# Optimization experiments

Hardware: AMD Instinct MI355X
Metric: run time of the kernel (lower is better)

Reference implementation:

```python
import jax, jax.numpy as jnp
import numpy as np

HIDDEN = 4096
N_HEADS = 16
HEAD_DIM = HIDDEN // N_HEADS  # 256
ROTARY_DIM = 64
ROPE_THETA = 10000.0


def _rope_cos_sin(positions):
    # positions: [S] int -> cos/sin: [S, ROTARY_DIM//2]
    inv_freq = 1.0 / (ROPE_THETA ** (jnp.arange(0, ROTARY_DIM, 2, dtype=jnp.float32) / ROTARY_DIM))
    angles = positions.astype(jnp.float32)[:, None] * inv_freq[None, :]
    return jnp.cos(angles), jnp.sin(angles)


def _apply_rope_interleaved(x, cos, sin):
    # x: [B, S, H, D]; rotate first ROTARY_DIM dims, GPT-J (non-neox) interleaved pairs
    xr = x[..., :ROTARY_DIM]
    x1 = xr[..., 0::2]
    x2 = xr[..., 1::2]
    c = cos[None, :, None, :]
    s = sin[None, :, None, :]
    o1 = x1 * c - x2 * s
    o2 = x1 * s + x2 * c
    rot = jnp.stack([o1, o2], axis=-1).reshape(xr.shape)
    return jnp.concatenate([rot, x[..., ROTARY_DIM:]], axis=-1)


def setup_inputs() -> dict:
    key = jax.random.key(0)
    k1, k2, k3 = jax.random.split(key, 3)
    B, S = 2, 2048
    hidden_states = jax.random.normal(k1, (B, S, HIDDEN), dtype=jnp.float32)
    positions = jnp.arange(S, dtype=jnp.int32)
    w_qkv = jax.random.normal(k2, (3 * HIDDEN, HIDDEN), dtype=jnp.float32) * 0.02
    w_out = jax.random.normal(k3, (HIDDEN, HIDDEN), dtype=jnp.float32) * 0.02
    return {"hidden_states": hidden_states, "positions": positions, "w_qkv": w_qkv, "w_out": w_out}


def reference(hidden_states, positions, w_qkv, w_out):
    B, S, H = hidden_states.shape
    qkv = jnp.einsum("bsh,oh->bso", hidden_states, w_qkv)  # [B,S,3H]
    q, k, v = jnp.split(qkv, 3, axis=-1)
    q = q.reshape(B, S, N_HEADS, HEAD_DIM)
    k = k.reshape(B, S, N_HEADS, HEAD_DIM)
    v = v.reshape(B, S, N_HEADS, HEAD_DIM)
    cos, sin = _rope_cos_sin(positions)
    q = _apply_rope_interleaved(q, cos, sin)
    k = _apply_rope_interleaved(k, cos, sin)
    scale = HEAD_DIM ** -0.5
    scores = jnp.einsum("bqhd,bkhd->bhqk", q, k) * scale  # [B,nh,S,S]
    causal = jnp.tril(jnp.ones((S, S), dtype=bool))
    scores = jnp.where(causal[None, None], scores, jnp.finfo(scores.dtype).min)
    probs = jax.nn.softmax(scores, axis=-1)
    attn = jnp.einsum("bhqk,bkhd->bqhd", probs, v).reshape(B, S, H)
    return jnp.einsum("bsh,oh->bso", attn, w_out)
```

## Files before the change

### kernel.cpp

```cpp
#include <hip/hip_runtime.h>

typedef __attribute__((ext_vector_type(8))) short short8;
typedef __attribute__((ext_vector_type(4))) float f32x4;

__device__ __forceinline__ unsigned short f2bf(float f) {
    union { float f; unsigned int u; } v; v.f = f;
    unsigned int u = v.u;
    unsigned int r = (u + 0x7FFFu + ((u >> 16) & 1u)) >> 16;
    return (unsigned short)r;
}
__device__ __forceinline__ float bf2f(unsigned short u) {
    union { unsigned int u; float f; } v; v.u = ((unsigned int)u) << 16;
    return v.f;
}
__device__ __forceinline__ void load_lds16(const void* g, void* l) {
    __builtin_amdgcn_global_load_lds(
        (const __attribute__((address_space(1))) void*)g,
        (__attribute__((address_space(3))) void*)l, 16, 0, 0);
}
#define BAR() asm volatile("s_barrier" ::: "memory")
#define WAITV(n) asm volatile("s_waitcnt vmcnt(" #n ")" ::: "memory")

__device__ __forceinline__ int swz(int o) { return o ^ ((o >> 3) & 0x70); }

__global__ __launch_bounds__(256) void conv_bf16(const float* __restrict__ in,
                                                 unsigned short* __restrict__ out, int n4) {
    int i = blockIdx.x * 256 + threadIdx.x;
    if (i >= n4) return;
    float4 v = ((const float4*)in)[i];
    ushort4 o;
    o.x = f2bf(v.x); o.y = f2bf(v.y); o.z = f2bf(v.z); o.w = f2bf(v.w);
    ((ushort4*)out)[i] = o;
}

template <bool OUT_BF16>
__global__ __launch_bounds__(512, 2) void gemm256(const unsigned short* __restrict__ A,
                                                  const unsigned short* __restrict__ B,
                                                  void* __restrict__ Cv,
                                                  int M, int N, int K, int NBN) {
    __shared__ __align__(16) char smem[131072];
    const int tid = threadIdx.x;
    const int lane = tid & 63, wv = tid >> 6;
    const int wm = wv >> 2, wn = wv & 3;
    const int fr = lane & 15, fo = (lane >> 4) * 8;

    const int nwg = gridDim.x, bid = blockIdx.x;
    const int q = nwg >> 3, r = nwg & 7, xcd = bid & 7, lid = bid >> 3;
    const int wg = (xcd < r ? xcd * (q + 1) : r * (q + 1) + (xcd - r) * q) + lid;
    const int bm = wg / NBN, bn = wg % NBN;

    const unsigned short* gA = A + (size_t)bm * 256 * K;
    const unsigned short* gB = B + (size_t)bn * 256 * K;

    int srow[2][2], scol[2][2];
#pragma unroll
    for (int h = 0; h < 2; ++h)
#pragma unroll
        for (int rr = 0; rr < 2; ++rr) {
            int o = h * 16384 + rr * 8192 + tid * 16;
            int osw = swz(o);
            srow[h][rr] = osw >> 7;
            scol[h][rr] = (osw & 127) >> 1;
        }

    f32x4 acc[8][4] = {};
    short8 a[4][2], b[4][2];

    auto STAGE = [&](const unsigned short* g, int regionBase, int h, int t) {
#pragma unroll
        for (int rr = 0; rr < 2; ++rr)
            load_lds16(g + (size_t)srow[h][rr] * K + t * 64 + scol[h][rr],
                       smem + regionBase + h * 16384 + rr * 8192 + tid * 16);
    };
    auto RDA = [&](int bufBase, int mh) {
#pragma unroll
        for (int mf = 0; mf < 4; ++mf)
#pragma unroll
            for (int ks = 0; ks < 2; ++ks) {
                int o = swz((wm * 128 + mh * 64 + mf * 16 + fr) * 128 + (ks * 32 + fo) * 2);
                a[mf][ks] = *(const short8*)(smem + bufBase + o);
            }
    };
    auto RDB = [&](int bufBase, int nh) {
#pragma unroll
        for (int jj = 0; jj < 2; ++jj)
#pragma unroll
            for (int ks = 0; ks < 2; ++ks) {
                int o = swz((wn * 64 + (nh * 2 + jj) * 16 + fr) * 128 + (ks * 32 + fo) * 2);
                b[nh * 2 + jj][ks] = *(const short8*)(smem + bufBase + 32768 + o);
            }
    };
    auto MM = [&](int mh, int nh) {
        __builtin_amdgcn_s_setprio(1);
#pragma unroll
        for (int mf = 0; mf < 4; ++mf)
#pragma unroll
            for (int jj = 0; jj < 2; ++jj)
#pragma unroll
                for (int ks = 0; ks < 2; ++ks)
                    acc[mh * 4 + mf][nh * 2 + jj] = __builtin_amdgcn_mfma_f32_16x16x32_bf16(
                        a[mf][ks], b[nh * 2 + jj][ks], acc[mh * 4 + mf][nh * 2 + jj], 0, 0, 0);
        __builtin_amdgcn_s_setprio(0);
    };

    const int A0 = 0, B0 = 32768, A1 = 65536, B1 = 98304;

    STAGE(gA, A0, 0, 0); STAGE(gA, A0, 1, 0);
    STAGE(gB, B0, 0, 0); STAGE(gB, B0, 1, 0);
    STAGE(gB, B1, 0, 1); STAGE(gB, B1, 1, 1);
    STAGE(gA, A1, 0, 1); STAGE(gA, A1, 1, 1);
    WAITV(8);
    BAR();
    RDA(A0, 0);
    RDB(A0, 0);

    const int NIT = K >> 7;
    for (int i = 0; i < NIT; ++i) {
        const bool last = (i == NIT - 1);
        const int t2 = 2 * i + 2, t3 = 2 * i + 3;
        RDB(A0, 1);
        MM(0, 0);
        if (i > 0) STAGE(gA, A1, 1, 2 * i + 1);
        BAR();
        MM(0, 1);
        RDA(A0, 1);
        BAR();
        MM(1, 1);
        if (!last) {
            STAGE(gB, B0, 0, t2);
            WAITV(2);
        } else {
            WAITV(0);
        }
        BAR();
        MM(1, 0);
        RDA(A1, 0); RDB(A1, 0);
        if (!last) { STAGE(gB, B0, 1, t2); STAGE(gA, A0, 0, t2); }
        BAR();
        RDB(A1, 1);
        MM(0, 0);
        if (!last) STAGE(gA, A0, 1, t2);
        BAR();
        MM(0, 1);
        RDA(A1, 1);
        BAR();
        MM(1, 1);
        if (!last) {
            STAGE(gB, B1, 0, t3);
            WAITV(2);
        }
        BAR();
        MM(1, 0);
        if (!last) {
            RDA(A0, 0); RDB(A0, 0);
            STAGE(gB, B1, 1, t3); STAGE(gA, A1, 0, t3);
        }
        BAR();
    }

    const size_t row0 = (size_t)bm * 256 + wm * 128 + ((lane >> 4) << 2);
    const int col0 = bn * 256 + wn * 64 + fr;
#pragma unroll
    for (int mf = 0; mf < 8; ++mf)
#pragma unroll
        for (int nf = 0; nf < 4; ++nf)
#pragma unroll
            for (int j = 0; j < 4; ++j) {
                size_t idx = (row0 + mf * 16 + j) * (size_t)N + col0 + nf * 16;
                if (OUT_BF16) ((unsigned short*)Cv)[idx] = f2bf(acc[mf][nf][j]);
                else          ((float*)Cv)[idx] = acc[mf][nf][j];
            }
}

__global__ __launch_bounds__(256) void rope_repack(const unsigned short* __restrict__ qkv,
                                                   const int* __restrict__ positions,
                                                   unsigned short* __restrict__ qp,
                                                   unsigned short* __restrict__ kp) {
    int r = blockIdx.x * 4 + (threadIdx.x >> 6);
    int h = r & 15, s = (r >> 4) & 2047, b = r >> 15;
    int d = (threadIdx.x & 63) * 4;
    const unsigned short* src = qkv + (size_t)(b * 2048 + s) * 12288 + h * 256 + d;
    ushort4 q = *(const ushort4*)src;
    ushort4 k = *(const ushort4*)(src + 4096);
    if (d < 64) {
        float pos = (float)positions[s];
        const float LF = 0.4152410118609203f;
        float i0 = (float)(d >> 1);
        float a0 = pos * exp2f(-i0 * LF);
        float a1 = pos * exp2f(-(i0 + 1.0f) * LF);
        float c0 = cosf(a0), s0 = sinf(a0), c1 = cosf(a1), s1 = sinf(a1);
        float qx = bf2f(q.x), qy = bf2f(q.y), qz = bf2f(q.z), qw = bf2f(q.w);
        q.x = f2bf(qx * c0 - qy * s0); q.y = f2bf(qx * s0 + qy * c0);
        q.z = f2bf(qz * c1 - qw * s1); q.w = f2bf(qz * s1 + qw * c1);
        float kx = bf2f(k.x), ky = bf2f(k.y), kz = bf2f(k.z), kw = bf2f(k.w);
        k.x = f2bf(kx * c0 - ky * s0); k.y = f2bf(kx * s0 + ky * c0);
        k.z = f2bf(kz * c1 - kw * s1); k.w = f2bf(kz * s1 + kw * c1);
    }
    size_t dst = ((size_t)((b * 16 + h) * 2048 + s)) * 256 + d;
    *(ushort4*)&qp[dst] = q;
    *(ushort4*)&kp[dst] = k;
}

__global__ __launch_bounds__(256) void v_transpose(const unsigned short* __restrict__ qkv,
                                                   unsigned short* __restrict__ vt) {
    int bid = blockIdx.x;
    int dt = bid & 3, st = (bid >> 2) & 31, bh = bid >> 7;
    int b = bh >> 4, h = bh & 15;
    __shared__ unsigned short t[64][72];
    int tid = threadIdx.x;
#pragma unroll
    for (int rep = 0; rep < 16; ++rep) {
        int idx = rep * 256 + tid;
        int r = idx >> 6, c = idx & 63;
        t[r][c] = qkv[(size_t)(b * 2048 + st * 64 + r) * 12288 + 8192 + h * 256 + dt * 64 + c];
    }
    __syncthreads();
#pragma unroll
    for (int rep = 0; rep < 16; ++rep) {
        int idx = rep * 256 + tid;
        int r = idx >> 6, c = idx & 63;
        vt[(size_t)(bh * 256 + dt * 64 + r) * 2048 + st * 64 + c] = t[c][r];
    }
}

__global__ __launch_bounds__(256) void attn_fwd(const unsigned short* __restrict__ Qp,
                                                const unsigned short* __restrict__ Kp,
                                                const unsigned short* __restrict__ Vt,
                                                unsigned short* __restrict__ Oa) {
    __shared__ __align__(16) unsigned short Ks[32 * 256];
    __shared__ __align__(16) unsigned short Vs[256 * 32];
    __shared__ __align__(16) unsigned short Ps[4][16 * 32];
    const int tid = threadIdx.x, lane = tid & 63, wv = tid >> 6;
    const int bh = blockIdx.x, qt = blockIdx.y;
    const int fr = lane & 15, fo = (lane >> 4) * 8;
    const unsigned short* Qb = Qp + (size_t)bh * 2048 * 256;
    const unsigned short* Kb = Kp + (size_t)bh * 2048 * 256;
    const unsigned short* Vb = Vt + (size_t)bh * 256 * 2048;
    const int qbase = qt * 64 + wv * 16;

    short8 qf[8];
#pragma unroll
    for (int c = 0; c < 8; ++c)
        qf[c] = *(const short8*)&Qb[(size_t)(qbase + fr) * 256 + c * 32 + fo];

    f32x4 o_acc[16] = {};
    float m_run[4] = {-1e30f, -1e30f, -1e30f, -1e30f};
    float l_run[4] = {0.f, 0.f, 0.f, 0.f};

    const int nkv = qt * 64 + 64;
    for (int kv0 = 0; kv0 < nkv; kv0 += 32) {
#pragma unroll
        for (int i = 0; i < 4; ++i) {
            int ob = (wv * 4 + i) * 1024 + lane * 16;
            int osw = ob ^ ((ob >> 5) & 0x70);
            int row = kv0 + (ob >> 9);
            load_lds16(&Kb[(size_t)row * 256 + ((osw & 511) >> 1)],
                       (char*)Ks + (wv * 4 + i) * 1024);
        }
#pragma unroll
        for (int i = 0; i < 4; ++i) {
            int ob = (wv * 4 + i) * 1024 + lane * 16;
            int osw = ob ^ ((((ob >> 6) ^ (ob >> 8)) & 3) << 4);
            int drow = ob >> 6;
            load_lds16(&Vb[(size_t)drow * 2048 + kv0 + ((osw & 63) >> 1)],
                       (char*)Vs + (wv * 4 + i) * 1024);
        }
        __syncthreads();

        f32x4 sc[2] = {};
#pragma unroll
        for (int t = 0; t < 2; ++t)
#pragma unroll
            for (int c = 0; c < 8; ++c) {
                int o = (t * 16 + fr) * 512 + (c * 32 + fo) * 2;
                o ^= (o >> 5) & 0x70;
                short8 kf = *(const short8*)((const char*)Ks + o);
                sc[t] = __builtin_amdgcn_mfma_f32_16x16x32_bf16(qf[c], kf, sc[t], 0, 0, 0);
            }

        float sv[2][4], pm[4];
#pragma unroll
        for (int j = 0; j < 4; ++j) {
            int qi = qbase + ((lane >> 4) << 2) + j;
#pragma unroll
            for (int t = 0; t < 2; ++t) {
                float x = sc[t][j] * 0.0625f;
                int kvi = kv0 + t * 16 + fr;
                sv[t][j] = (kvi > qi) ? -1e30f : x;
            }
            float p = fmaxf(sv[0][j], sv[1][j]);
#pragma unroll
            for (int off = 1; off < 16; off <<= 1)
                p = fmaxf(p, __shfl_xor(p, off));
            pm[j] = p;
        }
        bool need = (pm[0] > m_run[0] + 8.f) | (pm[1] > m_run[1] + 8.f) |
                    (pm[2] > m_run[2] + 8.f) | (pm[3] > m_run[3] + 8.f);
        if (__any(need)) {
#pragma unroll
            for (int j = 0; j < 4; ++j) {
                float mn = fmaxf(m_run[j], pm[j]);
                float al = __expf(m_run[j] - mn);
                m_run[j] = mn;
                l_run[j] *= al;
#pragma unroll
                for (int n = 0; n < 16; ++n) o_acc[n][j] *= al;
            }
        }
#pragma unroll
        for (int j = 0; j < 4; ++j) {
            float rs = 0.f;
#pragma unroll
            for (int t = 0; t < 2; ++t) {
                float p = __expf(sv[t][j] - m_run[j]);
                rs += p;
                Ps[wv][(((lane >> 4) << 2) + j) * 32 + t * 16 + fr] = f2bf(p);
            }
#pragma unroll
            for (int off = 1; off < 16; off <<= 1)
                rs += __shfl_xor(rs, off);
            l_run[j] += rs;
        }

        short8 pf = *(const short8*)&Ps[wv][fr * 32 + fo];
#pragma unroll
        for (int n = 0; n < 16; ++n) {
            int o = (n * 16 + fr) * 64 + fo * 2;
            o ^= (((o >> 6) ^ (o >> 8)) & 3) << 4;
            short8 vf = *(const short8*)((const char*)Vs + o);
            o_acc[n] = __builtin_amdgcn_mfma_f32_16x16x32_bf16(pf, vf, o_acc[n], 0, 0, 0);
        }
        __syncthreads();
    }

    const int b = bh >> 4, h = bh & 15;
#pragma unroll
    for (int j = 0; j < 4; ++j) {
        float inv = 1.0f / l_run[j];
        int qrow = qbase + ((lane >> 4) << 2) + j;
        size_t base = ((size_t)(b * 2048 + qrow)) * 4096 + h * 256;
#pragma unroll
        for (int n = 0; n < 16; ++n)
            Oa[base + n * 16 + fr] = f2bf(o_acc[n][j] * inv);
    }
}

extern "C" void kernel_launch(void* const* d_in, const int* in_sizes, int n_in,
                              void* d_out, int out_size, void* d_ws, size_t ws_size,
                              hipStream_t stream) {
    const float* hidden = (const float*)d_in[0];
    const int* positions = (const int*)d_in[1];
    const float* w_qkv = (const float*)d_in[2];
    const float* w_out = (const float*)d_in[3];
    float* out = (float*)d_out;

    const size_t MB32 = 33554432;
    char* ws = (char*)d_ws;
    unsigned short* hidden_bf = (unsigned short*)ws;
    unsigned short* wqkv_bf   = (unsigned short*)(ws + MB32);
    unsigned short* qkv_bf    = (unsigned short*)(ws + 4 * MB32);
    unsigned short* qp  = wqkv_bf;
    unsigned short* kp  = wqkv_bf + 16777216;
    unsigned short* vtp = wqkv_bf + 33554432;
    unsigned short* attn_bf = hidden_bf;
    unsigned short* wout_bf = qkv_bf;

    conv_bf16<<<16384, 256, 0, stream>>>(hidden, hidden_bf, 4194304);
    conv_bf16<<<49152, 256, 0, stream>>>(w_qkv, wqkv_bf, 12582912);

    gemm256<true><<<16 * 48, 512, 0, stream>>>(hidden_bf, wqkv_bf, qkv_bf, 4096, 12288, 4096, 48);

    rope_repack<<<16384, 256, 0, stream>>>(qkv_bf, positions, qp, kp);
    v_transpose<<<4096, 256, 0, stream>>>(qkv_bf, vtp);

    attn_fwd<<<dim3(32, 32), 256, 0, stream>>>(qp, kp, vtp, attn_bf);

    conv_bf16<<<16384, 256, 0, stream>>>(w_out, wout_bf, 4194304);
    gemm256<false><<<16 * 16, 512, 0, stream>>>(attn_bf, wout_bf, out, 4096, 4096, 4096, 16);
}
```

Before: 861.6 us.

## Double-buffer K/V tiles in attention kernel to overlap loads with compute

The attention kernel now keeps two LDS buffers for K and V tiles and issues async global-to-LDS loads for the next KV tile before computing on the current one. A partial vmcnt wait followed by a raw s_barrier replaces the full __syncthreads wait, so memory latency can overlap with the MFMA and softmax work. LDS use roughly doubles, which can lower occupancy. Correctness relies on the per-thread vmcnt accounting being right and on the barrier placement ordering the buffer reuse.

Result: slower. 880.6 us (+2.2%).

```diff
diff --git a/kernel.cpp b/kernel.cpp
--- a/kernel.cpp
+++ b/kernel.cpp
@@ -227,8 +227,8 @@
                                                 const unsigned short* __restrict__ Kp,
                                                 const unsigned short* __restrict__ Vt,
                                                 unsigned short* __restrict__ Oa) {
-    __shared__ __align__(16) unsigned short Ks[32 * 256];
-    __shared__ __align__(16) unsigned short Vs[256 * 32];
+    __shared__ __align__(16) unsigned short Ks[2][32 * 256];
+    __shared__ __align__(16) unsigned short Vs[2][256 * 32];
     __shared__ __align__(16) unsigned short Ps[4][16 * 32];
     const int tid = threadIdx.x, lane = tid & 63, wv = tid >> 6;
     const int bh = blockIdx.x, qt = blockIdx.y;
@@ -247,15 +247,15 @@
     float m_run[4] = {-1e30f, -1e30f, -1e30f, -1e30f};
     float l_run[4] = {0.f, 0.f, 0.f, 0.f};
 
-    const int nkv = qt * 64 + 64;
-    for (int kv0 = 0; kv0 < nkv; kv0 += 32) {
+    auto STAGE_T = [&](int t, int bsel) {
+        const int kv0 = t * 32;
 #pragma unroll
         for (int i = 0; i < 4; ++i) {
             int ob = (wv * 4 + i) * 1024 + lane * 16;
             int osw = ob ^ ((ob >> 5) & 0x70);
             int row = kv0 + (ob >> 9);
             load_lds16(&Kb[(size_t)row * 256 + ((osw & 511) >> 1)],
-                       (char*)Ks + (wv * 4 + i) * 1024);
+                       (char*)Ks[bsel] + (wv * 4 + i) * 1024);
         }
 #pragma unroll
         for (int i = 0; i < 4; ++i) {
@@ -263,19 +263,32 @@
             int osw = ob ^ ((((ob >> 6) ^ (ob >> 8)) & 3) << 4);
             int drow = ob >> 6;
             load_lds16(&Vb[(size_t)drow * 2048 + kv0 + ((osw & 63) >> 1)],
-                       (char*)Vs + (wv * 4 + i) * 1024);
-        }
-        __syncthreads();
+                       (char*)Vs[bsel] + (wv * 4 + i) * 1024);
+        }
+    };
+
+    const int nt = (qt * 64 + 64) >> 5;
+    STAGE_T(0, 0);
+    for (int t = 0; t < nt; ++t) {
+        const int bsel = t & 1;
+        const int kv0 = t * 32;
+        if (t + 1 < nt) {
+            STAGE_T(t + 1, bsel ^ 1);
+            WAITV(8);
+        } else {
+            WAITV(0);
+        }
+        BAR();
 
         f32x4 sc[2] = {};
 #pragma unroll
-        for (int t = 0; t < 2; ++t)
+        for (int tt = 0; tt < 2; ++tt)
 #pragma unroll
             for (int c = 0; c < 8; ++c) {
-                int o = (t * 16 + fr) * 512 + (c * 32 + fo) * 2;
+                int o = (tt * 16 + fr) * 512 + (c * 32 + fo) * 2;
                 o ^= (o >> 5) & 0x70;
-                short8 kf = *(const short8*)((const char*)Ks + o);
-                sc[t] = __builtin_amdgcn_mfma_f32_16x16x32_bf16(qf[c], kf, sc[t], 0, 0, 0);
+                short8 kf = *(const short8*)((const char*)Ks[bsel] + o);
+                sc[tt] = __builtin_amdgcn_mfma_f32_16x16x32_bf16(qf[c], kf, sc[tt], 0, 0, 0);
             }
 
         float sv[2][4], pm[4];
@@ -283,10 +296,10 @@
         for (int j = 0; j < 4; ++j) {
             int qi = qbase + ((lane >> 4) << 2) + j;
 #pragma unroll
-            for (int t = 0; t < 2; ++t) {
-                float x = sc[t][j] * 0.0625f;
-                int kvi = kv0 + t * 16 + fr;
-                sv[t][j] = (kvi > qi) ? -1e30f : x;
+            for (int tt = 0; tt < 2; ++tt) {
+                float x = sc[tt][j] * 0.0625f;
+                int kvi = kv0 + tt * 16 + fr;
+                sv[tt][j] = (kvi > qi) ? -1e30f : x;
             }
             float p = fmaxf(sv[0][j], sv[1][j]);
 #pragma unroll
@@ -311,10 +324,10 @@
         for (int j = 0; j < 4; ++j) {
             float rs = 0.f;
 #pragma unroll
-            for (int t = 0; t < 2; ++t) {
-                float p = __expf(sv[t][j] - m_run[j]);
+            for (int tt = 0; tt < 2; ++tt) {
+                float p = __expf(sv[tt][j] - m_run[j]);
                 rs += p;
-                Ps[wv][(((lane >> 4) << 2) + j) * 32 + t * 16 + fr] = f2bf(p);
+                Ps[wv][(((lane >> 4) << 2) + j) * 32 + tt * 16 + fr] = f2bf(p);
             }
 #pragma unroll
             for (int off = 1; off < 16; off <<= 1)
@@ -327,10 +340,10 @@
         for (int n = 0; n < 16; ++n) {
             int o = (n * 16 + fr) * 64 + fo * 2;
             o ^= (((o >> 6) ^ (o >> 8)) & 3) << 4;
-            short8 vf = *(const short8*)((const char*)Vs + o);
+            short8 vf = *(const short8*)((const char*)Vs[bsel] + o);
             o_acc[n] = __builtin_amdgcn_mfma_f32_16x16x32_bf16(pf, vf, o_acc[n], 0, 0, 0);
         }
-        __syncthreads();
+        BAR();
     }
 
     const int b = bh >> 4, h = bh & 15;
```
